# Optimization experiments

Hardware: AMD Instinct MI355X
Metric: run time of the kernel (lower is better)

The kernel has to match this reference:

```python
import jax, jax.numpy as jnp
import numpy as np

E = 256      # embedding_dim == value_dim
H = 8        # n_heads
DK = 64      # per-head q/k dim
DV = E // H  # per-head v dim = 32
LB = 32      # look_back
LF = 32      # look_forward
WIN = LB + LF + 1  # 65
NEG = -1e9


def setup_inputs() -> dict:
    key = jax.random.key(0)
    ks = jax.random.split(key, 8)
    B, S = 4, 8192
    s_in = 1.0 / np.sqrt(E)
    inp = {
        "x":        jax.random.normal(ks[0], (B, S, E), jnp.float32),
        "Wq":       jax.random.normal(ks[1], (E, H * DK), jnp.float32) * s_in,
        "bq":       jnp.zeros((H * DK,), jnp.float32),
        "Wk":       jax.random.normal(ks[2], (E, H * DK), jnp.float32) * s_in,
        "bk":       jnp.zeros((H * DK,), jnp.float32),
        "Wv":       jax.random.normal(ks[3], (E, H * DV), jnp.float32) * s_in,
        "bv":       jnp.zeros((H * DV,), jnp.float32),
        "Wo":       jax.random.normal(ks[4], (H * DV, E), jnp.float32) * s_in,
        "bo":       jnp.zeros((E,), jnp.float32),
        "rel_bias": jax.random.normal(ks[5], (H, WIN), jnp.float32) * 0.02,
        "ln1_g":    jnp.ones((E,), jnp.float32),
        "ln1_b":    jnp.zeros((E,), jnp.float32),
        "W_lin":    jax.random.normal(ks[6], (E, E), jnp.float32) * s_in,
        "b_lin":    jnp.zeros((E,), jnp.float32),
        "ln2_g":    jnp.ones((E,), jnp.float32),
        "ln2_b":    jnp.zeros((E,), jnp.float32),
    }
    return inp


def _layer_norm(x, g, b, eps=1e-5):
    m = jnp.mean(x, axis=-1, keepdims=True)
    v = jnp.var(x, axis=-1, keepdims=True)
    return (x - m) * jax.lax.rsqrt(v + eps) * g + b


def _local_rel_attention(x, Wq, bq, Wk, bk, Wv, bv, Wo, bo, rel_bias):
    B, S, _ = x.shape
    # project and split heads -> [B, H, S, d]
    q = (x @ Wq + bq).reshape(B, S, H, DK).transpose(0, 2, 1, 3)
    k = (x @ Wk + bk).reshape(B, S, H, DK).transpose(0, 2, 1, 3)
    v = (x @ Wv + bv).reshape(B, S, H, DV).transpose(0, 2, 1, 3)
    # pad keys/values along seq so window offsets become plain slices
    kp = jnp.pad(k, ((0, 0), (0, 0), (LB, LF), (0, 0)))
    vp = jnp.pad(v, ((0, 0), (0, 0), (LB, LF), (0, 0)))
    scale = 1.0 / np.sqrt(DK)
    scores = jnp.stack(
        [jnp.einsum("bhsd,bhsd->bhs", q, kp[:, :, w:w + S]) for w in range(WIN)],
        axis=-1,
    ) * scale
    scores = scores + rel_bias[None, :, None, :]
    # mask window entries that fall outside [0, S)
    key_pos = jnp.arange(S)[:, None] + jnp.arange(WIN)[None, :] - LB
    valid = (key_pos >= 0) & (key_pos < S)
    scores = jnp.where(valid[None, None], scores, NEG)
    p = jax.nn.softmax(scores, axis=-1)
    # banded PV: out[b,h,i,:] = sum_w p[b,h,i,w] * v_{i-LB+w}
    out = sum(p[..., w, None] * vp[:, :, w:w + S, :] for w in range(WIN))
    out = out.transpose(0, 2, 1, 3).reshape(B, S, H * DV)
    return out @ Wo + bo


def reference(x, Wq, bq, Wk, bk, Wv, bv, Wo, bo, rel_bias,
              ln1_g, ln1_b, W_lin, b_lin, ln2_g, ln2_b):
    res = _local_rel_attention(x, Wq, bq, Wk, bk, Wv, bv, Wo, bo, rel_bias)
    xs = _layer_norm(x + res, ln1_g, ln1_b)
    res = jax.nn.relu(xs @ W_lin + b_lin)
    xs = _layer_norm(xs + res, ln2_g, ln2_b)
    return xs
```

## Files before the change

### kernel.cpp

```cpp
#include <hip/hip_runtime.h>
#include <math.h>

#define S_LEN 8192
#define NB 4
#define NH 8
#define BSROWS (NB * S_LEN)

typedef __bf16 bf16x8 __attribute__((ext_vector_type(8)));
typedef float f32x4 __attribute__((ext_vector_type(4)));
typedef unsigned short u16;
typedef const __attribute__((address_space(1))) void* as1cv;
typedef __attribute__((address_space(3))) void* as3v;

__device__ __forceinline__ u16 f2bf(float f) {
    union { float f; unsigned int u; } v; v.f = f;
    unsigned int r = v.u + 0x7FFFu + ((v.u >> 16) & 1u);
    return (u16)(r >> 16);
}

__device__ __forceinline__ void gload16(const void* g, void* l) {
    __builtin_amdgcn_global_load_lds((as1cv)g, (as3v)l, 16, 0, 0);
}

__device__ __forceinline__ bf16x8 lds_b8(const u16* base, int byteoff) {
    return *reinterpret_cast<const bf16x8*>(reinterpret_cast<const char*>(base) + byteoff);
}

template<bool RELU, bool BF16OUT>
__global__ __launch_bounds__(256, 2)
void gemm_bf16(const u16* __restrict__ A, const u16* __restrict__ Wt,
               const float* __restrict__ bias, void* __restrict__ Cv,
               int N, int nbx)
{
    __shared__ u16 As[128 * 64];
    __shared__ u16 Bs[128 * 64];

    const int t = threadIdx.x;
    const int wv = t >> 6, ln = t & 63;

    const int nwg = gridDim.x;
    const int qq = nwg >> 3;
    const int swz = (blockIdx.x & 7) * qq + (blockIdx.x >> 3);
    const int by = swz / nbx, bx = swz % nbx;
    const int rbase = by * 128, cbase = bx * 128;

    const int wr = wv >> 1, wc = wv & 1;
    const int frow = ln & 15, fk = ln >> 4;

    f32x4 acc[4][4];
#pragma unroll
    for (int i = 0; i < 4; ++i)
#pragma unroll
        for (int j = 0; j < 4; ++j) acc[i][j] = f32x4{0.f, 0.f, 0.f, 0.f};

    const int srow_b = (ln >> 3);
    const int scb    = ln & 7;

    for (int k0 = 0; k0 < 256; k0 += 64) {
#pragma unroll
        for (int r = 0; r < 4; ++r) {
            const int rowA = r * 32 + wv * 8 + srow_b;
            const int cbs = scb ^ (rowA & 7);
            gload16(A + (size_t)(rbase + rowA) * 256 + k0 + cbs * 8,
                    As + r * 2048 + wv * 512);
            gload16(Wt + (size_t)(cbase + rowA) * 256 + k0 + cbs * 8,
                    Bs + r * 2048 + wv * 512);
        }
        __syncthreads();

        bf16x8 af[4][2], bfr[4][2];
#pragma unroll
        for (int mi = 0; mi < 4; ++mi)
#pragma unroll
            for (int kk = 0; kk < 2; ++kk) {
                const int row = wr * 64 + mi * 16 + frow;
                const int cb = (kk * 4 + fk) ^ (row & 7);
                af[mi][kk] = lds_b8(As, row * 128 + cb * 16);
            }
#pragma unroll
        for (int ni = 0; ni < 4; ++ni)
#pragma unroll
            for (int kk = 0; kk < 2; ++kk) {
                const int row = wc * 64 + ni * 16 + frow;
                const int cb = (kk * 4 + fk) ^ (row & 7);
                bfr[ni][kk] = lds_b8(Bs, row * 128 + cb * 16);
            }
#pragma unroll
        for (int mi = 0; mi < 4; ++mi)
#pragma unroll
            for (int ni = 0; ni < 4; ++ni)
#pragma unroll
                for (int kk = 0; kk < 2; ++kk)
                    acc[mi][ni] = __builtin_amdgcn_mfma_f32_16x16x32_bf16(
                        af[mi][kk], bfr[ni][kk], acc[mi][ni], 0, 0, 0);
        __syncthreads();
    }

    float cbias[4];
#pragma unroll
    for (int ni = 0; ni < 4; ++ni)
        cbias[ni] = bias[cbase + wc * 64 + ni * 16 + frow];

#pragma unroll
    for (int mi = 0; mi < 4; ++mi) {
        const int row0 = rbase + wr * 64 + mi * 16 + fk * 4;
#pragma unroll
        for (int ni = 0; ni < 4; ++ni) {
            const int col = cbase + wc * 64 + ni * 16 + frow;
#pragma unroll
            for (int j = 0; j < 4; ++j) {
                float v = acc[mi][ni][j] + cbias[ni];
                if (RELU) v = fmaxf(v, 0.f);
                if (BF16OUT)
                    ((u16*)Cv)[(size_t)(row0 + j) * N + col] = f2bf(v);
                else
                    ((float*)Cv)[(size_t)(row0 + j) * N + col] = v;
            }
        }
    }
}

__global__ __launch_bounds__(256, 3)
void attn_mfma(const u16* __restrict__ qkv, const u16* __restrict__ vt,
               const float* __restrict__ rel, u16* __restrict__ ob)
{
    __shared__ u16 Ks[128 * 64];
    __shared__ u16 Qs[64 * 64];
    __shared__ u16 Vts[32 * 128];
    __shared__ u16 Ps[4][16 * 104];
    __shared__ float rbs[72];

    const int t = threadIdx.x, wv = t >> 6, ln = t & 63;
    const int bh = blockIdx.y, b = bh >> 3, h = bh & 7;
    const int i0 = blockIdx.x * 64;

#pragma unroll
    for (int r = 0; r < 4; ++r) {
        const int row = r * 32 + wv * 8 + (ln >> 3);
        const int cbs = (ln & 7) ^ (row & 7);
        int pos = i0 - 32 + row;
        pos = pos < 0 ? 0 : (pos >= S_LEN ? S_LEN - 1 : pos);
        const long long grow = (long long)b * S_LEN + pos;
        gload16((const char*)qkv + grow * 2560 + 1024 + h * 128 + cbs * 16,
                Ks + r * 2048 + wv * 512);
    }
#pragma unroll
    for (int r = 0; r < 2; ++r) {
        const int row = r * 32 + wv * 8 + (ln >> 3);
        const int cbs = (ln & 7) ^ (row & 7);
        gload16((const char*)qkv + ((size_t)(b * S_LEN + i0 + row)) * 2560 + h * 128 + cbs * 16,
                Qs + r * 2048 + wv * 512);
    }
#pragma unroll
    for (int r = 0; r < 2; ++r) {
        const int row = r * 16 + wv * 4 + (ln >> 4);
        const int cbs = (ln & 15) ^ (row & 15);
        long long off = (long long)(i0 - 32) * 2 + cbs * 16;
        off = off < 0 ? 0 : (off > (long long)(S_LEN * 2 - 16) ? (long long)(S_LEN * 2 - 16) : off);
        gload16((const char*)vt + ((size_t)bh * 32 + row) * (S_LEN * 2) + off,
                Vts + r * 2048 + wv * 512);
    }
    if (t < 65) rbs[t] = rel[h * 65 + t];
    __syncthreads();

    const int frow = ln & 15, fk = ln >> 4, g = fk;

    bf16x8 aq[2];
    const int qrow = wv * 16 + frow;
#pragma unroll
    for (int kk = 0; kk < 2; ++kk) {
        const int cb = (kk * 4 + fk) ^ (qrow & 7);
        aq[kk] = lds_b8(Qs, qrow * 128 + cb * 16);
    }
    f32x4 sacc[5];
#pragma unroll
    for (int ni = 0; ni < 5; ++ni) {
        sacc[ni] = f32x4{0.f, 0.f, 0.f, 0.f};
        const int krow = wv * 16 + ni * 16 + frow;
#pragma unroll
        for (int kk = 0; kk < 2; ++kk) {
            const int cb = (kk * 4 + fk) ^ (krow & 7);
            bf16x8 bk = lds_b8(Ks, krow * 128 + cb * 16);
            sacc[ni] = __builtin_amdgcn_mfma_f32_16x16x32_bf16(aq[kk], bk, sacc[ni], 0, 0, 0);
        }
    }

    float p[5][4];
#pragma unroll
    for (int j = 0; j < 4; ++j) {
        const int qloc = g * 4 + j;
        const int iq = i0 + wv * 16 + qloc;
        float mx = -1e30f;
#pragma unroll
        for (int ni = 0; ni < 5; ++ni) {
            const int w = ni * 16 + frow - qloc;
            const long long pos = (long long)iq - 32 + w;
            const bool valid = (w >= 0) & (w <= 64) & (pos >= 0) & (pos < S_LEN);
            const int wc2 = w < 0 ? 0 : (w > 64 ? 64 : w);
            const float s = valid ? fmaf(sacc[ni][j], 0.125f, rbs[wc2]) : -1e9f;
            p[ni][j] = s;
            mx = fmaxf(mx, s);
        }
        mx = fmaxf(mx, __shfl_xor(mx, 1));
        mx = fmaxf(mx, __shfl_xor(mx, 2));
        mx = fmaxf(mx, __shfl_xor(mx, 4));
        mx = fmaxf(mx, __shfl_xor(mx, 8));
        float sum = 0.f;
#pragma unroll
        for (int ni = 0; ni < 5; ++ni) {
            const float e = __expf(p[ni][j] - mx);
            p[ni][j] = e; sum += e;
        }
        sum += __shfl_xor(sum, 1);
        sum += __shfl_xor(sum, 2);
        sum += __shfl_xor(sum, 4);
        sum += __shfl_xor(sum, 8);
        const float inv = 1.f / sum;
#pragma unroll
        for (int ni = 0; ni < 5; ++ni) p[ni][j] *= inv;
    }

    u16* Pw = &Ps[wv][0];
    {
        const int zr = ln >> 2, zc = 80 + (ln & 3) * 4;
        *reinterpret_cast<uint2*>(Pw + zr * 104 + zc) = uint2{0u, 0u};
    }
#pragma unroll
    for (int ni = 0; ni < 5; ++ni)
#pragma unroll
        for (int j = 0; j < 4; ++j)
            Pw[(g * 4 + j) * 104 + ni * 16 + frow] = f2bf(p[ni][j]);

    __syncthreads();

    f32x4 oacc[2];
    oacc[0] = f32x4{0.f, 0.f, 0.f, 0.f};
    oacc[1] = f32x4{0.f, 0.f, 0.f, 0.f};
#pragma unroll
    for (int kk = 0; kk < 3; ++kk) {
        bf16x8 bp = lds_b8(Pw, frow * 208 + kk * 64 + fk * 16);
#pragma unroll
        for (int mi = 0; mi < 2; ++mi) {
            const int dv = mi * 16 + frow;
            const int cbv = ((wv * 2 + kk * 4 + fk) & 15) ^ (dv & 15);
            bf16x8 av = lds_b8(Vts, dv * 256 + cbv * 16);
            oacc[mi] = __builtin_amdgcn_mfma_f32_16x16x32_bf16(av, bp, oacc[mi], 0, 0, 0);
        }
    }

    const int iq = i0 + wv * 16 + frow;
#pragma unroll
    for (int mi = 0; mi < 2; ++mi)
#pragma unroll
        for (int j = 0; j < 4; ++j) {
            const int dv = mi * 16 + g * 4 + j;
            ob[((size_t)(b * S_LEN + iq)) * 256 + h * 32 + dv] = f2bf(oacc[mi][j]);
        }
}

template<bool DUAL>
__global__ __launch_bounds__(256, 4)
void add_ln(const float* __restrict__ a, const float* __restrict__ r,
            const float* __restrict__ g, const float* __restrict__ be,
            float* __restrict__ o, u16* __restrict__ ob16)
{
    const int row = blockIdx.x * 4 + (threadIdx.x >> 6);
    const int lane = threadIdx.x & 63;
    const size_t base = (size_t)row * 256 + lane * 4;

    const float4 va = *reinterpret_cast<const float4*>(&a[base]);
    const float4 vr = *reinterpret_cast<const float4*>(&r[base]);
    const float v0 = va.x + vr.x, v1 = va.y + vr.y;
    const float v2 = va.z + vr.z, v3 = va.w + vr.w;

    float sum = v0 + v1 + v2 + v3;
#pragma unroll
    for (int off = 32; off; off >>= 1) sum += __shfl_xor(sum, off);
    const float mean = sum * (1.f / 256.f);

    const float d0 = v0 - mean, d1 = v1 - mean, d2 = v2 - mean, d3 = v3 - mean;
    float ss = d0 * d0 + d1 * d1 + d2 * d2 + d3 * d3;
#pragma unroll
    for (int off = 32; off; off >>= 1) ss += __shfl_xor(ss, off);
    const float rs = rsqrtf(ss * (1.f / 256.f) + 1e-5f);

    const float4 vg = *reinterpret_cast<const float4*>(&g[lane * 4]);
    const float4 vb = *reinterpret_cast<const float4*>(&be[lane * 4]);
    float4 out;
    out.x = d0 * rs * vg.x + vb.x;
    out.y = d1 * rs * vg.y + vb.y;
    out.z = d2 * rs * vg.z + vb.z;
    out.w = d3 * rs * vg.w + vb.w;
    *reinterpret_cast<float4*>(&o[base]) = out;
    if (DUAL) {
        uint2 pk;
        pk.x = (unsigned)f2bf(out.x) | ((unsigned)f2bf(out.y) << 16);
        pk.y = (unsigned)f2bf(out.z) | ((unsigned)f2bf(out.w) << 16);
        *reinterpret_cast<uint2*>(&ob16[base]) = pk;
    }
}

__global__ void cvt_x_bf16(const float* __restrict__ in, u16* __restrict__ out)
{
    const int i = blockIdx.x * 256 + threadIdx.x;
    const float4* p = reinterpret_cast<const float4*>(in) + (size_t)i * 2;
    const float4 a = p[0], c = p[1];
    uint4 u;
    u.x = (unsigned)f2bf(a.x) | ((unsigned)f2bf(a.y) << 16);
    u.y = (unsigned)f2bf(a.z) | ((unsigned)f2bf(a.w) << 16);
    u.z = (unsigned)f2bf(c.x) | ((unsigned)f2bf(c.y) << 16);
    u.w = (unsigned)f2bf(c.z) | ((unsigned)f2bf(c.w) << 16);
    *(reinterpret_cast<uint4*>(out) + i) = u;
}

__global__ void cvt_wt(const float* __restrict__ w, u16* __restrict__ wt,
                       int N, int roff)
{
    const int n = blockIdx.x, k = threadIdx.x;
    wt[(size_t)(n + roff) * 256 + k] = f2bf(w[(size_t)k * N + n]);
}

__global__ void bias_cat(const float* __restrict__ bq, const float* __restrict__ bk,
                         const float* __restrict__ bv, float* __restrict__ o)
{
    const int i = blockIdx.x * 256 + threadIdx.x;
    o[i] = i < 512 ? bq[i] : (i < 1024 ? bk[i - 512] : bv[i - 1024]);
}

__global__ __launch_bounds__(256, 4)
void v_transpose(const u16* __restrict__ qkv, u16* __restrict__ vt)
{
    __shared__ u16 L[32][264];
    const int bh = blockIdx.y, b = bh >> 3, h = bh & 7;
    const int s0 = blockIdx.x * 256;
    const int t = threadIdx.x;

    const u16* src = qkv + ((size_t)(b * S_LEN + s0 + t)) * 1280 + 1024 + h * 32;
#pragma unroll
    for (int c = 0; c < 4; ++c) {
        uint4 val = *reinterpret_cast<const uint4*>(src + c * 8);
        L[c * 8 + 0][t] = (u16)(val.x & 0xFFFF); L[c * 8 + 1][t] = (u16)(val.x >> 16);
        L[c * 8 + 2][t] = (u16)(val.y & 0xFFFF); L[c * 8 + 3][t] = (u16)(val.y >> 16);
        L[c * 8 + 4][t] = (u16)(val.z & 0xFFFF); L[c * 8 + 5][t] = (u16)(val.z >> 16);
        L[c * 8 + 6][t] = (u16)(val.w & 0xFFFF); L[c * 8 + 7][t] = (u16)(val.w >> 16);
    }
    __syncthreads();
    const int dv = t >> 3, ch = t & 7;
    u16* dst = vt + ((size_t)bh * 32 + dv) * S_LEN + s0 + ch * 32;
#pragma unroll
    for (int c = 0; c < 4; ++c) {
        uint4 u;
        const u16* lp = &L[dv][ch * 32 + c * 8];
        u.x = (unsigned)lp[0] | ((unsigned)lp[1] << 16);
        u.y = (unsigned)lp[2] | ((unsigned)lp[3] << 16);
        u.z = (unsigned)lp[4] | ((unsigned)lp[5] << 16);
        u.w = (unsigned)lp[6] | ((unsigned)lp[7] << 16);
        *reinterpret_cast<uint4*>(dst + c * 8) = u;
    }
}

extern "C" void kernel_launch(void* const* d_in, const int* in_sizes, int n_in,
                              void* d_out, int out_size, void* d_ws, size_t ws_size,
                              hipStream_t stream)
{
    const float* x   = (const float*)d_in[0];
    const float* Wq  = (const float*)d_in[1];
    const float* bq  = (const float*)d_in[2];
    const float* Wk  = (const float*)d_in[3];
    const float* bk  = (const float*)d_in[4];
    const float* Wv  = (const float*)d_in[5];
    const float* bv  = (const float*)d_in[6];
    const float* Wo  = (const float*)d_in[7];
    const float* bo  = (const float*)d_in[8];
    const float* rel = (const float*)d_in[9];
    const float* g1  = (const float*)d_in[10];
    const float* b1  = (const float*)d_in[11];
    const float* Wl  = (const float*)d_in[12];
    const float* bl  = (const float*)d_in[13];
    const float* g2  = (const float*)d_in[14];
    const float* b2  = (const float*)d_in[15];
    float* out = (float*)d_out;

    u16* qkvb  = (u16*)d_ws;
    u16* vt    = qkvb  + (size_t)BSROWS * 1280;
    u16* xb    = vt    + (size_t)BSROWS * 256;
    u16* wqkvt = xb    + (size_t)BSROWS * 256;
    u16* wot   = wqkvt + 1280 * 256;
    u16* wlt   = wot   + 256 * 256;
    float* bqkv = (float*)(wlt + 256 * 256);

    float* tmp = (float*)qkvb;
    float* xs  = (float*)qkvb + (size_t)BSROWS * 256;
    float* lin = tmp;
    u16*   xsb   = vt;
    u16*   attnb = xb;

    dim3 blk(256);

    cvt_x_bf16<<<4096, blk, 0, stream>>>(x, xb);
    cvt_wt<<<512, blk, 0, stream>>>(Wq, wqkvt, 512, 0);
    cvt_wt<<<512, blk, 0, stream>>>(Wk, wqkvt, 512, 512);
    cvt_wt<<<256, blk, 0, stream>>>(Wv, wqkvt, 256, 1024);
    cvt_wt<<<256, blk, 0, stream>>>(Wo, wot, 256, 0);
    cvt_wt<<<256, blk, 0, stream>>>(Wl, wlt, 256, 0);
    bias_cat<<<5, blk, 0, stream>>>(bq, bk, bv, bqkv);

    gemm_bf16<false, true><<<dim3(10 * 256), blk, 0, stream>>>(xb, wqkvt, bqkv, qkvb, 1280, 10);

    v_transpose<<<dim3(32, 32), blk, 0, stream>>>(qkvb, vt);

    attn_mfma<<<dim3(S_LEN / 64, NB * NH), blk, 0, stream>>>(qkvb, vt, rel, attnb);

    gemm_bf16<false, false><<<dim3(2 * 256), blk, 0, stream>>>(attnb, wot, bo, tmp, 256, 2);
    add_ln<true><<<dim3(BSROWS / 4), blk, 0, stream>>>(tmp, x, g1, b1, xs, xsb);
    gemm_bf16<true, false><<<dim3(2 * 256), blk, 0, stream>>>(xsb, wlt, bl, lin, 256, 2);
    add_ln<false><<<dim3(BSROWS / 4), blk, 0, stream>>>(lin, xs, g2, b2, out, nullptr);
}
```

Measured before the change: 248.7 us.

## Fuse V transpose into QKV GEMM epilogue and merge prep kernels

Result: faster. 234.4 us (-5.7%).

```diff
diff --git a/kernel.cpp b/kernel.cpp
--- a/kernel.cpp
+++ b/kernel.cpp
@@ -26,11 +26,11 @@
     return *reinterpret_cast<const bf16x8*>(reinterpret_cast<const char*>(base) + byteoff);
 }
 
-template<bool RELU, bool BF16OUT>
+template<bool RELU, bool BF16OUT, bool VFUSE>
 __global__ __launch_bounds__(256, 2)
 void gemm_bf16(const u16* __restrict__ A, const u16* __restrict__ Wt,
                const float* __restrict__ bias, void* __restrict__ Cv,
-               int N, int nbx)
+               u16* __restrict__ vtout, int N, int nbx)
 {
     __shared__ u16 As[128 * 64];
     __shared__ u16 Bs[128 * 64];
@@ -100,6 +100,27 @@
 #pragma unroll
     for (int ni = 0; ni < 4; ++ni)
         cbias[ni] = bias[cbase + wc * 64 + ni * 16 + frow];
+
+    if (VFUSE && cbase >= 1024) {
+#pragma unroll
+        for (int mi = 0; mi < 4; ++mi) {
+            const int row0 = rbase + wr * 64 + mi * 16 + fk * 4;
+            const int b = row0 >> 13, s = row0 & 8191;
+#pragma unroll
+            for (int ni = 0; ni < 4; ++ni) {
+                const int vcol = cbase - 1024 + wc * 64 + ni * 16 + frow;
+                const int h = vcol >> 5, dv = vcol & 31;
+                uint2 pk;
+                pk.x = (unsigned)f2bf(acc[mi][ni][0] + cbias[ni]) |
+                       ((unsigned)f2bf(acc[mi][ni][1] + cbias[ni]) << 16);
+                pk.y = (unsigned)f2bf(acc[mi][ni][2] + cbias[ni]) |
+                       ((unsigned)f2bf(acc[mi][ni][3] + cbias[ni]) << 16);
+                *reinterpret_cast<uint2*>(
+                    vtout + ((size_t)((b * 8 + h) * 32 + dv)) * S_LEN + s) = pk;
+            }
+        }
+        return;
+    }
 
 #pragma unroll
     for (int mi = 0; mi < 4; ++mi) {
@@ -300,62 +321,46 @@
     }
 }
 
-__global__ void cvt_x_bf16(const float* __restrict__ in, u16* __restrict__ out)
+__global__ void prep_inputs(const float* __restrict__ x,
+                            const float* __restrict__ Wq, const float* __restrict__ Wk,
+                            const float* __restrict__ Wv, const float* __restrict__ Wo,
+                            const float* __restrict__ Wl,
+                            const float* __restrict__ bq, const float* __restrict__ bk,
+                            const float* __restrict__ bv,
+                            u16* __restrict__ xb, u16* __restrict__ wqkvt,
+                            u16* __restrict__ wot, u16* __restrict__ wlt,
+                            float* __restrict__ bqkv)
 {
-    const int i = blockIdx.x * 256 + threadIdx.x;
-    const float4* p = reinterpret_cast<const float4*>(in) + (size_t)i * 2;
-    const float4 a = p[0], c = p[1];
-    uint4 u;
-    u.x = (unsigned)f2bf(a.x) | ((unsigned)f2bf(a.y) << 16);
-    u.y = (unsigned)f2bf(a.z) | ((unsigned)f2bf(a.w) << 16);
-    u.z = (unsigned)f2bf(c.x) | ((unsigned)f2bf(c.y) << 16);
-    u.w = (unsigned)f2bf(c.z) | ((unsigned)f2bf(c.w) << 16);
-    *(reinterpret_cast<uint4*>(out) + i) = u;
-}
-
-__global__ void cvt_wt(const float* __restrict__ w, u16* __restrict__ wt,
-                       int N, int roff)
-{
-    const int n = blockIdx.x, k = threadIdx.x;
-    wt[(size_t)(n + roff) * 256 + k] = f2bf(w[(size_t)k * N + n]);
-}
-
-__global__ void bias_cat(const float* __restrict__ bq, const float* __restrict__ bk,
-                         const float* __restrict__ bv, float* __restrict__ o)
-{
-    const int i = blockIdx.x * 256 + threadIdx.x;
-    o[i] = i < 512 ? bq[i] : (i < 1024 ? bk[i - 512] : bv[i - 1024]);
-}
-
-__global__ __launch_bounds__(256, 4)
-void v_transpose(const u16* __restrict__ qkv, u16* __restrict__ vt)
-{
-    __shared__ u16 L[32][264];
-    const int bh = blockIdx.y, b = bh >> 3, h = bh & 7;
-    const int s0 = blockIdx.x * 256;
-    const int t = threadIdx.x;
-
-    const u16* src = qkv + ((size_t)(b * S_LEN + s0 + t)) * 1280 + 1024 + h * 32;
-#pragma unroll
-    for (int c = 0; c < 4; ++c) {
-        uint4 val = *reinterpret_cast<const uint4*>(src + c * 8);
-        L[c * 8 + 0][t] = (u16)(val.x & 0xFFFF); L[c * 8 + 1][t] = (u16)(val.x >> 16);
-        L[c * 8 + 2][t] = (u16)(val.y & 0xFFFF); L[c * 8 + 3][t] = (u16)(val.y >> 16);
-        L[c * 8 + 4][t] = (u16)(val.z & 0xFFFF); L[c * 8 + 5][t] = (u16)(val.z >> 16);
-        L[c * 8 + 6][t] = (u16)(val.w & 0xFFFF); L[c * 8 + 7][t] = (u16)(val.w >> 16);
-    }
-    __syncthreads();
-    const int dv = t >> 3, ch = t & 7;
-    u16* dst = vt + ((size_t)bh * 32 + dv) * S_LEN + s0 + ch * 32;
-#pragma unroll
-    for (int c = 0; c < 4; ++c) {
+    const int bid = blockIdx.x, t = threadIdx.x;
+    if (bid < 4096) {
+        const int i = bid * 256 + t;
+        const float4* p = reinterpret_cast<const float4*>(x) + (size_t)i * 2;
+        const float4 a = p[0], c = p[1];
         uint4 u;
-        const u16* lp = &L[dv][ch * 32 + c * 8];
-        u.x = (unsigned)lp[0] | ((unsigned)lp[1] << 16);
-        u.y = (unsigned)lp[2] | ((unsigned)lp[3] << 16);
-        u.z = (unsigned)lp[4] | ((unsigned)lp[5] << 16);
-        u.w = (unsigned)lp[6] | ((unsigned)lp[7] << 16);
-        *reinterpret_cast<uint4*>(dst + c * 8) = u;
+        u.x = (unsigned)f2bf(a.x) | ((unsigned)f2bf(a.y) << 16);
+        u.y = (unsigned)f2bf(a.z) | ((unsigned)f2bf(a.w) << 16);
+        u.z = (unsigned)f2bf(c.x) | ((unsigned)f2bf(c.y) << 16);
+        u.w = (unsigned)f2bf(c.z) | ((unsigned)f2bf(c.w) << 16);
+        *(reinterpret_cast<uint4*>(xb) + i) = u;
+    } else if (bid < 4096 + 512) {
+        const int n = bid - 4096;
+        wqkvt[(size_t)n * 256 + t] = f2bf(Wq[(size_t)t * 512 + n]);
+    } else if (bid < 4096 + 1024) {
+        const int n = bid - (4096 + 512);
+        wqkvt[(size_t)(n + 512) * 256 + t] = f2bf(Wk[(size_t)t * 512 + n]);
+    } else if (bid < 4096 + 1280) {
+        const int n = bid - (4096 + 1024);
+        wqkvt[(size_t)(n + 1024) * 256 + t] = f2bf(Wv[(size_t)t * 256 + n]);
+    } else if (bid < 4096 + 1536) {
+        const int n = bid - (4096 + 1280);
+        wot[(size_t)n * 256 + t] = f2bf(Wo[(size_t)t * 256 + n]);
+    } else if (bid < 4096 + 1792) {
+        const int n = bid - (4096 + 1536);
+        wlt[(size_t)n * 256 + t] = f2bf(Wl[(size_t)t * 256 + n]);
+    } else {
+        const int i = (bid - (4096 + 1792)) * 256 + t;
+        if (i < 1280)
+            bqkv[i] = i < 512 ? bq[i] : (i < 1024 ? bk[i - 512] : bv[i - 1024]);
     }
 }
 
@@ -397,22 +402,18 @@
 
     dim3 blk(256);
 
-    cvt_x_bf16<<<4096, blk, 0, stream>>>(x, xb);
-    cvt_wt<<<512, blk, 0, stream>>>(Wq, wqkvt, 512, 0);
-    cvt_wt<<<512, blk, 0, stream>>>(Wk, wqkvt, 512, 512);
-    cvt_wt<<<256, blk, 0, stream>>>(Wv, wqkvt, 256, 1024);
-    cvt_wt<<<256, blk, 0, stream>>>(Wo, wot, 256, 0);
-    cvt_wt<<<256, blk, 0, stream>>>(Wl, wlt, 256, 0);
-    bias_cat<<<5, blk, 0, stream>>>(bq, bk, bv, bqkv);
-
-    gemm_bf16<false, true><<<dim3(10 * 256), blk, 0, stream>>>(xb, wqkvt, bqkv, qkvb, 1280, 10);
-
-    v_transpose<<<dim3(32, 32), blk, 0, stream>>>(qkvb, vt);
+    prep_inputs<<<4096 + 1792 + 5, blk, 0, stream>>>(
+        x, Wq, Wk, Wv, Wo, Wl, bq, bk, bv, xb, wqkvt, wot, wlt, bqkv);
+
+    gemm_bf16<false, true, true><<<dim3(10 * 256), blk, 0, stream>>>(
+        xb, wqkvt, bqkv, qkvb, vt, 1280, 10);
 
     attn_mfma<<<dim3(S_LEN / 64, NB * NH), blk, 0, stream>>>(qkvb, vt, rel, attnb);
 
-    gemm_bf16<false, false><<<dim3(2 * 256), blk, 0, stream>>>(attnb, wot, bo, tmp, 256, 2);
+    gemm_bf16<false, false, false><<<dim3(2 * 256), blk, 0, stream>>>(
+        attnb, wot, bo, tmp, nullptr, 256, 2);
     add_ln<true><<<dim3(BSROWS / 4), blk, 0, stream>>>(tmp, x, g1, b1, xs, xsb);
-    gemm_bf16<true, false><<<dim3(2 * 256), blk, 0, stream>>>(xsb, wlt, bl, lin, 256, 2);
+    gemm_bf16<true, false, false><<<dim3(2 * 256), blk, 0, stream>>>(
+        xsb, wlt, bl, lin, nullptr, 256, 2);
     add_ln<false><<<dim3(BSROWS / 4), blk, 0, stream>>>(lin, xs, g2, b2, out, nullptr);
 }
```
